# Kernel tuning notes

Measured on AMD Instinct MI355X. Metric: run time of the kernel, lower is better.

Reference implementation:

```python
import jax, jax.numpy as jnp
import numpy as np

N_NODES = 50000
N_EDGES = 800000
F_IN, C1, C2 = 128, 100, 4
NEG_SLOPE = 0.2  # PyG GATConv default LeakyReLU slope


def setup_inputs() -> dict:
    key = jax.random.key(0)
    ks = jax.random.split(key, 10)
    def glorot(k, shape):
        fan = sum(shape)
        return jax.random.normal(k, shape, jnp.float32) * jnp.sqrt(2.0 / fan)
    return {
        "x": jax.random.normal(ks[0], (N_NODES, F_IN), jnp.float32),
        "edge_index": jax.random.randint(ks[1], (2, N_EDGES), 0, N_NODES, jnp.int64),
        "W1": glorot(ks[2], (F_IN, C1)),
        "att_src1": glorot(ks[3], (1, C1)),
        "att_dst1": glorot(ks[4], (1, C1)),
        "b1": jnp.zeros((C1,), jnp.float32),
        "W2": glorot(ks[5], (C1, C2)),
        "att_src2": glorot(ks[6], (1, C2)),
        "att_dst2": glorot(ks[7], (1, C2)),
        "b2": jnp.zeros((C2,), jnp.float32),
    }


def _gat_conv(x, edge_index, W, att_src, att_dst, bias):
    """PyG GATConv (heads=1, concat=True, add_self_loops=True), eval mode."""
    n = x.shape[0]
    # add self loops
    loop = jnp.arange(n, dtype=edge_index.dtype)
    src = jnp.concatenate([edge_index[0], loop])
    dst = jnp.concatenate([edge_index[1], loop])
    h = x @ W                                   # [N, C]
    a_src = (h * att_src[0]).sum(-1)            # [N]
    a_dst = (h * att_dst[0]).sum(-1)            # [N]
    e = jax.nn.leaky_relu(a_src[src] + a_dst[dst], NEG_SLOPE)  # [E+N]
    # segment softmax over destination neighborhoods
    m = jax.ops.segment_max(e, dst, num_segments=n)            # [N]
    w = jnp.exp(e - m[dst])
    denom = jax.ops.segment_sum(w, dst, num_segments=n)        # [N]
    alpha = w / denom[dst]                                     # [E+N]
    msg = h[src] * alpha[:, None]                              # [E+N, C]
    out = jax.ops.segment_sum(msg, dst, num_segments=n)        # [N, C]
    return out + bias


def reference(x, edge_index, W1, att_src1, att_dst1, b1, W2, att_src2, att_dst2, b2):
    h = _gat_conv(x, edge_index, W1, att_src1, att_dst1, b1)
    h = jax.nn.relu(h)  # dropout is identity in eval mode
    h = _gat_conv(h, edge_index, W2, att_src2, att_dst2, b2)
    return jax.nn.log_softmax(h, axis=1)
```

## Files before the change

### kernel.cpp

```cpp
#include <hip/hip_runtime.h>
#include <math.h>

#define N_NODES 50000
#define N_EDGES 800000
#define F_IN 128
#define C1 100
#define C1D 50
#define C2 4
#define NEG 0.2f
#define NB_ZERO 196
#define NB_E4 782
#define DEGCAP 64

typedef __attribute__((ext_vector_type(8))) short bf16x8;
typedef __attribute__((ext_vector_type(4))) float f32x4;

__device__ __forceinline__ float leaky(float v) { return v > 0.f ? v : NEG * v; }
__device__ __forceinline__ unsigned f2bf(float f) {
    unsigned u = __float_as_uint(f);
    u += 0x7FFF + ((u >> 16) & 1);
    return u >> 16;
}
__device__ __forceinline__ float bf_lo(unsigned g) { return __uint_as_float(g << 16); }
__device__ __forceinline__ float bf_hi(unsigned g) { return __uint_as_float(g & 0xFFFF0000u); }

__global__ __launch_bounds__(256) void k_prep(int* __restrict__ cnt, const float* __restrict__ W1,
                                              unsigned short* __restrict__ W1bf) {
    int i = blockIdx.x * 256 + threadIdx.x;
    if (i < N_NODES) cnt[i] = 0;
    if (i < 12800) {
        int k = i / 100, n = i - k * 100;
        W1bf[n * 128 + k] = (unsigned short)f2bf(W1[i]);
    } else if (i < 12800 + 12 * 128) {
        int e = i - 12800;
        int n = 100 + (e >> 7), k = e & 127;
        W1bf[n * 128 + k] = 0;
    }
}

__global__ __attribute__((amdgpu_waves_per_eu(1, 3))) __launch_bounds__(256)
void k_gemm_scatter(const float* __restrict__ x, const unsigned short* __restrict__ W1bf,
                    const float* __restrict__ as1, const float* __restrict__ ad1,
                    unsigned* __restrict__ h1b, float* __restrict__ a_src1,
                    float* __restrict__ a_dst1, const int* __restrict__ ei,
                    int* __restrict__ cnt, int* __restrict__ slots) {
    int half = blockIdx.x >> 1;
    if (blockIdx.x & 1) {
        int i = half * 256 + threadIdx.x;
        if (i >= N_EDGES / 4) return;
        int4 s4 = *(const int4*)(ei + i * 4);
        int4 d4 = *(const int4*)(ei + N_EDGES + i * 4);
        int sl;
        sl = atomicAdd(&cnt[d4.x], 1); if (sl < DEGCAP) slots[d4.x * DEGCAP + sl] = s4.x;
        sl = atomicAdd(&cnt[d4.y], 1); if (sl < DEGCAP) slots[d4.y * DEGCAP + sl] = s4.y;
        sl = atomicAdd(&cnt[d4.z], 1); if (sl < DEGCAP) slots[d4.z * DEGCAP + sl] = s4.z;
        sl = atomicAdd(&cnt[d4.w], 1); if (sl < DEGCAP) slots[d4.w * DEGCAP + sl] = s4.w;
        return;
    }
    int tid = threadIdx.x;
    int node0 = half * 64;
    int wave = tid >> 6, lane = tid & 63;
    int mrow = lane & 15;
    int quad = lane >> 4;
    int na = node0 + wave * 16 + mrow;
    bool vrow = na < N_NODES;
    const float* px = x + (long)na * F_IN + quad * 8;

    bf16x8 afr[4];
#pragma unroll
    for (int kc = 0; kc < 4; ++kc) {
        float4 v0 = make_float4(0.f, 0.f, 0.f, 0.f), v1 = v0;
        if (vrow) {
            v0 = *(const float4*)(px + kc * 32);
            v1 = *(const float4*)(px + kc * 32 + 4);
        }
        bf16x8 t;
        t[0] = (short)f2bf(v0.x); t[1] = (short)f2bf(v0.y);
        t[2] = (short)f2bf(v0.z); t[3] = (short)f2bf(v0.w);
        t[4] = (short)f2bf(v1.x); t[5] = (short)f2bf(v1.y);
        t[6] = (short)f2bf(v1.z); t[7] = (short)f2bf(v1.w);
        afr[kc] = t;
    }

    f32x4 acc[7];
#pragma unroll
    for (int nt = 0; nt < 7; ++nt) {
        const unsigned short* pb = W1bf + (nt * 16 + mrow) * 128 + quad * 8;
        f32x4 a = {0.f, 0.f, 0.f, 0.f};
#pragma unroll
        for (int kc = 0; kc < 4; ++kc) {
            bf16x8 bfr = *(const bf16x8*)(pb + kc * 32);
            a = __builtin_amdgcn_mfma_f32_16x16x32_bf16(afr[kc], bfr, a, 0, 0, 0);
        }
        acc[nt] = a;
    }

    float ps[4] = {0.f, 0.f, 0.f, 0.f}, pd[4] = {0.f, 0.f, 0.f, 0.f};
#pragma unroll
    for (int nt = 0; nt < 7; ++nt) {
        int col = nt * 16 + mrow;
        float av = 0.f, dv = 0.f;
        if (col < C1) { av = as1[col]; dv = ad1[col]; }
#pragma unroll
        for (int r = 0; r < 4; ++r) {
            ps[r] += acc[nt][r] * av;
            pd[r] += acc[nt][r] * dv;
        }
    }
#pragma unroll
    for (int r = 0; r < 4; ++r) {
#pragma unroll
        for (int off = 1; off < 16; off <<= 1) {
            ps[r] += __shfl_xor(ps[r], off);
            pd[r] += __shfl_xor(pd[r], off);
        }
    }
    if (mrow == 0) {
#pragma unroll
        for (int r = 0; r < 4; ++r) {
            int n = node0 + wave * 16 + quad * 4 + r;
            if (n < N_NODES) { a_src1[n] = ps[r]; a_dst1[n] = pd[r]; }
        }
    }

#pragma unroll
    for (int nt = 0; nt < 7; ++nt) {
#pragma unroll
        for (int r = 0; r < 4; ++r) {
            float v = acc[nt][r];
            float o = __shfl_xor(v, 1);
            int col = nt * 16 + mrow;
            int n = node0 + wave * 16 + quad * 4 + r;
            if ((mrow & 1) == 0 && col < C1 && n < N_NODES) {
                unsigned pk = f2bf(v) | (f2bf(o) << 16);
                h1b[(long)n * C1D + (col >> 1)] = pk;
            }
        }
    }
}

__global__ __launch_bounds__(256) void k_agg1(const unsigned* __restrict__ h1b, const float* __restrict__ a_src,
                                              const float* __restrict__ a_dst, const int* __restrict__ cnt,
                                              const int* __restrict__ slots, const float* __restrict__ b1,
                                              const float* __restrict__ W2, const float* __restrict__ as2,
                                              const float* __restrict__ ad2, float4* __restrict__ h2,
                                              float* __restrict__ a_src2, float* __restrict__ a_dst2) {
    __shared__ float sW2[C1 * C2];
    __shared__ float sB1[C1];
    int tid = threadIdx.x;
    for (int f = tid; f < C1 * C2; f += 256) sW2[f] = W2[f];
    if (tid < C1) sB1[tid] = b1[tid];
    __syncthreads();
    int wave = tid >> 6, lane = tid & 63;
    int d = blockIdx.x * 4 + wave;
    if (d >= N_NODES) return;
    int cn = min(cnt[d], DEGCAP);
    float ad = a_dst[d];
    int c = lane;
    bool act = c < C1D;

    float wself = __expf(leaky(a_src[d] + ad));
    unsigned gs = act ? h1b[(long)d * C1D + c] : 0u;
    float accL = wself * bf_lo(gs), accH = wself * bf_hi(gs);
    float lsum = (lane == 0) ? wself : 0.f;

    int sreg = 0; float wreg = 0.f;
    if (lane < cn) {
        sreg = slots[d * DEGCAP + lane];
        wreg = __expf(leaky(a_src[sreg] + ad));
        lsum += wreg;
    }
    unsigned g[8];
#pragma unroll
    for (int i = 0; i < 8; ++i) {
        int sv = __shfl(sreg, i);
        g[i] = act ? h1b[(long)sv * C1D + c] : 0u;
    }
    int jj = 0;
    for (; jj + 8 <= cn; jj += 8) {
        unsigned cb[8];
#pragma unroll
        for (int i = 0; i < 8; ++i) cb[i] = g[i];
#pragma unroll
        for (int i = 0; i < 8; ++i) {
            int sv = __shfl(sreg, jj + 8 + i);
            g[i] = act ? h1b[(long)sv * C1D + c] : 0u;
        }
#pragma unroll
        for (int i = 0; i < 8; ++i) {
            float w = __shfl(wreg, jj + i);
            accL += w * bf_lo(cb[i]); accH += w * bf_hi(cb[i]);
        }
    }
#pragma unroll
    for (int i = 0; i < 7; ++i) {
        if (jj + i < cn) {
            float w = __shfl(wreg, jj + i);
            accL += w * bf_lo(g[i]); accH += w * bf_hi(g[i]);
        }
    }

    for (int off = 32; off; off >>= 1) lsum += __shfl_xor(lsum, off);
    float invl = 1.f / lsum;
    float p0 = 0.f, p1 = 0.f, p2 = 0.f, p3 = 0.f;
    if (act) {
        float v0 = fmaxf(accL * invl + sB1[2 * c], 0.f);
        float v1 = fmaxf(accH * invl + sB1[2 * c + 1], 0.f);
        const float* w0 = &sW2[(2 * c) * 4];
        p0 = v0 * w0[0] + v1 * w0[4];
        p1 = v0 * w0[1] + v1 * w0[5];
        p2 = v0 * w0[2] + v1 * w0[6];
        p3 = v0 * w0[3] + v1 * w0[7];
    }
    for (int off = 32; off; off >>= 1) {
        p0 += __shfl_xor(p0, off);
        p1 += __shfl_xor(p1, off);
        p2 += __shfl_xor(p2, off);
        p3 += __shfl_xor(p3, off);
    }
    if (lane == 0) {
        h2[d] = make_float4(p0, p1, p2, p3);
        a_src2[d] = p0 * as2[0] + p1 * as2[1] + p2 * as2[2] + p3 * as2[3];
        a_dst2[d] = p0 * ad2[0] + p1 * ad2[1] + p2 * ad2[2] + p3 * ad2[3];
    }
}

__global__ __launch_bounds__(256) void k_agg2(const float4* __restrict__ h2, const float* __restrict__ a_src,
                                              const float* __restrict__ a_dst, const int* __restrict__ cnt,
                                              const int* __restrict__ slots, const float* __restrict__ b2,
                                              float4* __restrict__ out) {
    int wave = threadIdx.x >> 6, lane = threadIdx.x & 63;
    int grp = lane >> 4, li = lane & 15;
    int d = blockIdx.x * 16 + wave * 4 + grp;
    if (d >= N_NODES) return;
    int cn = min(cnt[d], DEGCAP);
    float ad = a_dst[d];
    float l = 0.f, a0 = 0.f, a1 = 0.f, a2 = 0.f, a3 = 0.f;
    if (li == 0) {
        float w = __expf(leaky(a_src[d] + ad));
        float4 hv = h2[d];
        l = w; a0 = w * hv.x; a1 = w * hv.y; a2 = w * hv.z; a3 = w * hv.w;
    }
    for (int j = li; j < cn; j += 16) {
        int s = slots[d * DEGCAP + j];
        float w = __expf(leaky(a_src[s] + ad));
        l += w;
        float4 hv = h2[s];
        a0 += w * hv.x; a1 += w * hv.y; a2 += w * hv.z; a3 += w * hv.w;
    }
#pragma unroll
    for (int off = 8; off; off >>= 1) {
        l += __shfl_xor(l, off);
        a0 += __shfl_xor(a0, off);
        a1 += __shfl_xor(a1, off);
        a2 += __shfl_xor(a2, off);
        a3 += __shfl_xor(a3, off);
    }
    if (li == 0) {
        float invl = 1.f / l;
        float v0 = a0 * invl + b2[0];
        float v1 = a1 * invl + b2[1];
        float v2 = a2 * invl + b2[2];
        float v3 = a3 * invl + b2[3];
        float mm = fmaxf(fmaxf(v0, v1), fmaxf(v2, v3));
        float ls = logf(__expf(v0 - mm) + __expf(v1 - mm) + __expf(v2 - mm) + __expf(v3 - mm)) + mm;
        out[d] = make_float4(v0 - ls, v1 - ls, v2 - ls, v3 - ls);
    }
}

extern "C" void kernel_launch(void* const* d_in, const int* in_sizes, int n_in,
                              void* d_out, int out_size, void* d_ws, size_t ws_size,
                              hipStream_t stream) {
    const float* x   = (const float*)d_in[0];
    const int*   ei  = (const int*)d_in[1];
    const float* W1  = (const float*)d_in[2];
    const float* as1 = (const float*)d_in[3];
    const float* ad1 = (const float*)d_in[4];
    const float* b1  = (const float*)d_in[5];
    const float* W2  = (const float*)d_in[6];
    const float* as2 = (const float*)d_in[7];
    const float* ad2 = (const float*)d_in[8];
    const float* b2  = (const float*)d_in[9];
    float4* out = (float4*)d_out;

    char* w = (char*)d_ws;
    unsigned* h1b    = (unsigned*)(w + 0);
    float*    a_src1 = (float*)(w + 10000000);
    float*    a_dst1 = (float*)(w + 10200000);
    float4*   h2     = (float4*)(w + 10400000);
    float*    a_src2 = (float*)(w + 11200000);
    float*    a_dst2 = (float*)(w + 11400000);
    int*      cnt    = (int*)(w + 11600000);
    int*      slots  = (int*)(w + 11800000);
    unsigned short* W1bf = (unsigned short*)(w + 24600000);

    k_prep<<<NB_ZERO, 256, 0, stream>>>(cnt, W1, W1bf);
    k_gemm_scatter<<<2 * NB_E4, 256, 0, stream>>>(x, W1bf, as1, ad1, h1b, a_src1, a_dst1,
                                                  ei, cnt, slots);
    k_agg1<<<(N_NODES + 3) / 4, 256, 0, stream>>>(h1b, a_src1, a_dst1, cnt, slots, b1, W2, as2, ad2,
                                                  h2, a_src2, a_dst2);
    k_agg2<<<(N_NODES + 15) / 16, 256, 0, stream>>>(h2, a_src2, a_dst2, cnt, slots, b2, out);
}
```

Before: 181.7 us.

## Split aggregation wave into two half-waves each gathering 8-byte bf16 rows

The layer-1 aggregation now has each lane load 4 bf16 channels (uint2) and splits the 64-lane wave into two halves that process alternating neighbor edges. The two halves' partial sums are combined with a cross-half shuffle at the end. Previously 14 of 64 lanes sat idle; now 25 of every 32 lanes are active and each load is wider, so fewer load instructions are issued per edge. The cost is an extra cross-half reduction and unaligned-size rows (100 bytes, 8-byte aligned), which may slightly reduce coalescing.

```diff
diff --git a/kernel.cpp b/kernel.cpp
--- a/kernel.cpp
+++ b/kernel.cpp
@@ -156,61 +156,75 @@
     if (d >= N_NODES) return;
     int cn = min(cnt[d], DEGCAP);
     float ad = a_dst[d];
-    int c = lane;
-    bool act = c < C1D;
-
-    float wself = __expf(leaky(a_src[d] + ad));
-    unsigned gs = act ? h1b[(long)d * C1D + c] : 0u;
-    float accL = wself * bf_lo(gs), accH = wself * bf_hi(gs);
-    float lsum = (lane == 0) ? wself : 0.f;
+    int h = lane >> 5, li = lane & 31;
+    bool act = li < 25;
 
     int sreg = 0; float wreg = 0.f;
     if (lane < cn) {
         sreg = slots[d * DEGCAP + lane];
         wreg = __expf(leaky(a_src[sreg] + ad));
-        lsum += wreg;
-    }
-    unsigned g[8];
-#pragma unroll
-    for (int i = 0; i < 8; ++i) {
-        int sv = __shfl(sreg, i);
-        g[i] = act ? h1b[(long)sv * C1D + c] : 0u;
+    }
+    float lsum = (lane < cn) ? wreg : 0.f;
+    float wself = __expf(leaky(a_src[d] + ad));
+    if (lane == 0) lsum += wself;
+
+    float acc[4] = {0.f, 0.f, 0.f, 0.f};
+    if (h == 0 && act) {
+        uint2 gv = *(const uint2*)(h1b + (long)d * C1D + 2 * li);
+        acc[0] = wself * bf_lo(gv.x); acc[1] = wself * bf_hi(gv.x);
+        acc[2] = wself * bf_lo(gv.y); acc[3] = wself * bf_hi(gv.y);
+    }
+
+    uint2 g[4];
+#pragma unroll
+    for (int i = 0; i < 4; ++i) {
+        int sv = __shfl(sreg, 2 * i + h);
+        g[i] = act ? *(const uint2*)(h1b + (long)sv * C1D + 2 * li) : make_uint2(0u, 0u);
     }
     int jj = 0;
     for (; jj + 8 <= cn; jj += 8) {
-        unsigned cb[8];
-#pragma unroll
-        for (int i = 0; i < 8; ++i) cb[i] = g[i];
-#pragma unroll
-        for (int i = 0; i < 8; ++i) {
-            int sv = __shfl(sreg, jj + 8 + i);
-            g[i] = act ? h1b[(long)sv * C1D + c] : 0u;
-        }
-#pragma unroll
-        for (int i = 0; i < 8; ++i) {
-            float w = __shfl(wreg, jj + i);
-            accL += w * bf_lo(cb[i]); accH += w * bf_hi(cb[i]);
-        }
-    }
-#pragma unroll
-    for (int i = 0; i < 7; ++i) {
-        if (jj + i < cn) {
-            float w = __shfl(wreg, jj + i);
-            accL += w * bf_lo(g[i]); accH += w * bf_hi(g[i]);
-        }
-    }
+        uint2 c0 = g[0], c1 = g[1], c2 = g[2], c3 = g[3];
+#pragma unroll
+        for (int i = 0; i < 4; ++i) {
+            int sv = __shfl(sreg, jj + 8 + 2 * i + h);
+            g[i] = act ? *(const uint2*)(h1b + (long)sv * C1D + 2 * li) : make_uint2(0u, 0u);
+        }
+        float w0 = __shfl(wreg, jj + 0 + h);
+        float w1 = __shfl(wreg, jj + 2 + h);
+        float w2 = __shfl(wreg, jj + 4 + h);
+        float w3 = __shfl(wreg, jj + 6 + h);
+        acc[0] += w0 * bf_lo(c0.x); acc[1] += w0 * bf_hi(c0.x);
+        acc[2] += w0 * bf_lo(c0.y); acc[3] += w0 * bf_hi(c0.y);
+        acc[0] += w1 * bf_lo(c1.x); acc[1] += w1 * bf_hi(c1.x);
+        acc[2] += w1 * bf_lo(c1.y); acc[3] += w1 * bf_hi(c1.y);
+        acc[0] += w2 * bf_lo(c2.x); acc[1] += w2 * bf_hi(c2.x);
+        acc[2] += w2 * bf_lo(c2.y); acc[3] += w2 * bf_hi(c2.y);
+        acc[0] += w3 * bf_lo(c3.x); acc[1] += w3 * bf_hi(c3.x);
+        acc[2] += w3 * bf_lo(c3.y); acc[3] += w3 * bf_hi(c3.y);
+    }
+#pragma unroll
+    for (int i = 0; i < 4; ++i) {
+        int e = jj + 2 * i + h;
+        if (e < cn) {
+            float w = __shfl(wreg, e);
+            acc[0] += w * bf_lo(g[i].x); acc[1] += w * bf_hi(g[i].x);
+            acc[2] += w * bf_lo(g[i].y); acc[3] += w * bf_hi(g[i].y);
+        }
+    }
+#pragma unroll
+    for (int k = 0; k < 4; ++k) acc[k] += __shfl_xor(acc[k], 32);
 
     for (int off = 32; off; off >>= 1) lsum += __shfl_xor(lsum, off);
     float invl = 1.f / lsum;
     float p0 = 0.f, p1 = 0.f, p2 = 0.f, p3 = 0.f;
-    if (act) {
-        float v0 = fmaxf(accL * invl + sB1[2 * c], 0.f);
-        float v1 = fmaxf(accH * invl + sB1[2 * c + 1], 0.f);
-        const float* w0 = &sW2[(2 * c) * 4];
-        p0 = v0 * w0[0] + v1 * w0[4];
-        p1 = v0 * w0[1] + v1 * w0[5];
-        p2 = v0 * w0[2] + v1 * w0[6];
-        p3 = v0 * w0[3] + v1 * w0[7];
+    if (h == 0 && act) {
+#pragma unroll
+        for (int k = 0; k < 4; ++k) {
+            int ch = 4 * li + k;
+            float v = fmaxf(acc[k] * invl + sB1[ch], 0.f);
+            const float* wr = &sW2[ch * 4];
+            p0 += v * wr[0]; p1 += v * wr[1]; p2 += v * wr[2]; p3 += v * wr[3];
+        }
     }
     for (int off = 32; off; off >>= 1) {
         p0 += __shfl_xor(p0, off);
```

Measured after the change: 188.4 us. +3.7%, slower.
